# Performance work log

Hardware: AMD Instinct MI355X
Metric: run time of the kernel (lower is better)

Reference implementation:

```python
import jax, jax.numpy as jnp
import numpy as np

N, E = 50000, 800000          # nodes, edges
IN, H1, D1 = 128, 8, 32       # gcn1: 8 heads x 32 -> concat 256
HID1 = H1 * D1                # 256
HID2 = 128                    # gcn2: 1 head x 128
FC1, OUT = 512, 1
NEG_SLOPE = 0.2


def _nrm(k, shape, s=0.05):
    return jax.random.normal(k, shape, jnp.float32) * s


def setup_inputs() -> dict:
    key = jax.random.key(0)
    ks = jax.random.split(key, 16)
    return {
        "x": jax.random.normal(ks[0], (N, IN), jnp.float32),
        "edge_index": jax.random.randint(ks[1], (2, E), 0, N, dtype=jnp.int32),
        # gcn1 params
        "W1": _nrm(ks[2], (IN, H1 * D1)),
        "att_src1": _nrm(ks[3], (H1, D1)),
        "att_dst1": _nrm(ks[4], (H1, D1)),
        "b1": jnp.zeros((HID1,), jnp.float32),
        # gcn2 params (1 head)
        "W2": _nrm(ks[5], (HID1, HID2)),
        "att_src2": _nrm(ks[6], (1, HID2)),
        "att_dst2": _nrm(ks[7], (1, HID2)),
        "b2": jnp.zeros((HID2,), jnp.float32),
        # fc head
        "fcW1": _nrm(ks[8], (HID2, FC1)),
        "fcb1": jnp.zeros((FC1,), jnp.float32),
        "fcW2": _nrm(ks[9], (FC1, OUT)),
        "fcb2": jnp.zeros((OUT,), jnp.float32),
    }


def gat_layer(x, src, dst, W, a_src, a_dst, b, heads, dim):
    """PyG GATConv (eval mode): gather -> segment-softmax over dst -> scatter."""
    n = x.shape[0]
    h = (x @ W).reshape(n, heads, dim)                     # [N,H,D]
    a_s = jnp.einsum('nhd,hd->nh', h, a_src)               # [N,H]
    a_d = jnp.einsum('nhd,hd->nh', h, a_dst)
    e = jax.nn.leaky_relu(a_s[src] + a_d[dst], NEG_SLOPE)  # [E,H]
    m = jax.ops.segment_max(e, dst, num_segments=n)        # [N,H]
    m = jnp.where(jnp.isfinite(m), m, 0.0)                 # empty segments
    ex = jnp.exp(e - m[dst])
    denom = jax.ops.segment_sum(ex, dst, num_segments=n)
    alpha = ex / (denom[dst] + 1e-16)                      # [E,H]
    out = jax.ops.segment_sum(h[src] * alpha[:, :, None], dst, num_segments=n)
    return out.reshape(n, heads * dim) + b, alpha


def reference(x, edge_index, W1, att_src1, att_dst1, b1,
              W2, att_src2, att_dst2, b2, fcW1, fcb1, fcW2, fcb2):
    src, dst = edge_index[0], edge_index[1]
    x1, alpha1 = gat_layer(x, src, dst, W1, att_src1, att_dst1, b1, H1, D1)
    x1 = jax.nn.elu(x1)
    x2, alpha2 = gat_layer(x1, src, dst, W2, att_src2, att_dst2, b2, 1, HID2)
    x2 = jax.nn.relu(x2)
    h = jax.nn.relu(x2 @ fcW1 + fcb1)
    out = h @ fcW2 + fcb2                                  # [N,1]
    return out, alpha1, alpha2
```

## Files before the change

kernel.cpp:

```cpp
#include <hip/hip_runtime.h>
#include <hip/hip_bf16.h>
#include <hip/hip_fp8.h>
#include <math.h>

#define NN 50000
#define EE 800000
#define IN_DIM 128
#define H1 8
#define D1 32
#define HID1 256
#define HID2 128
#define FC1 512
#define NEG_SLOPE 0.2f

typedef short v8s __attribute__((ext_vector_type(8)));
typedef float v4f __attribute__((ext_vector_type(4)));
typedef float v2f __attribute__((ext_vector_type(2)));
typedef unsigned int v4u __attribute__((ext_vector_type(4)));

__device__ __forceinline__ float bf2f(unsigned short u) {
    unsigned int x = ((unsigned int)u) << 16;
    return __uint_as_float(x);
}
__device__ __forceinline__ unsigned short f2bf(float v) {
    __hip_bfloat16 h = __float2bfloat16(v);
    return *(unsigned short*)&h;
}
__device__ __forceinline__ unsigned char f2f8(float v) {
    __hip_fp8_e4m3 t(v);
    return (unsigned char)t.__x;
}
__device__ __forceinline__ float f8tof(unsigned char u) {
    __hip_fp8_e4m3 t;
    t.__x = (__hip_fp8_storage_t)u;
    return (float)t;
}

__device__ __forceinline__ void f8x4(unsigned int w, float& f0, float& f1, float& f2, float& f3) {
#if __has_builtin(__builtin_amdgcn_cvt_pk_f32_fp8)
    v2f lo = __builtin_amdgcn_cvt_pk_f32_fp8((int)w, false);
    v2f hi = __builtin_amdgcn_cvt_pk_f32_fp8((int)w, true);
    f0 = lo[0]; f1 = lo[1]; f2 = hi[0]; f3 = hi[1];
#else
    f0 = f8tof((unsigned char)(w & 0xff));
    f1 = f8tof((unsigned char)((w >> 8) & 0xff));
    f2 = f8tof((unsigned char)((w >> 16) & 0xff));
    f3 = f8tof((unsigned char)(w >> 24));
#endif
}


__global__ void hist_kernel(const int* __restrict__ dst, int* __restrict__ counts) {
    int e = blockIdx.x * blockDim.x + threadIdx.x;
    if (e < EE) atomicAdd(&counts[dst[e]], 1);
}

__global__ __launch_bounds__(256) void scan_a_kernel(const int* __restrict__ counts,
                                                     int* __restrict__ excl,
                                                     int* __restrict__ bsum, int n) {
    __shared__ int wsum[4];
    int tid = threadIdx.x;
    int base = blockIdx.x * 1024 + tid * 4;
    int v0 = 0, v1 = 0, v2 = 0, v3 = 0;
    if (base + 3 < n) {
        int4 t = *(const int4*)(counts + base);
        v0 = t.x; v1 = t.y; v2 = t.z; v3 = t.w;
    } else {
        if (base + 0 < n) v0 = counts[base + 0];
        if (base + 1 < n) v1 = counts[base + 1];
        if (base + 2 < n) v2 = counts[base + 2];
        if (base + 3 < n) v3 = counts[base + 3];
    }
    int tot = v0 + v1 + v2 + v3;
    int lane = tid & 63;
    int w = tid >> 6;
    int x = tot;
    #pragma unroll
    for (int off = 1; off < 64; off <<= 1) {
        int y = __shfl_up(x, off);
        if (lane >= off) x += y;
    }
    if (lane == 63) wsum[w] = x;
    __syncthreads();
    int woff = 0;
    for (int i = 0; i < w; i++) woff += wsum[i];
    int et = woff + x - tot;
    if (base + 0 < n) excl[base + 0] = et;
    if (base + 1 < n) excl[base + 1] = et + v0;
    if (base + 2 < n) excl[base + 2] = et + v0 + v1;
    if (base + 3 < n) excl[base + 3] = et + v0 + v1 + v2;
    if (tid == 255) bsum[blockIdx.x] = woff + x;
}

__global__ __launch_bounds__(64) void scan_b_kernel(int* __restrict__ bsum,
                                                    int* __restrict__ row_ptr, int nb, int n) {
    int lane = threadIdx.x;
    int v = (lane < nb) ? bsum[lane] : 0;
    int x = v;
    #pragma unroll
    for (int off = 1; off < 64; off <<= 1) {
        int y = __shfl_up(x, off);
        if (lane >= off) x += y;
    }
    if (lane < nb) bsum[lane] = x - v;
    if (lane == 63) row_ptr[n] = x;
}

__global__ __launch_bounds__(256) void scan_c_kernel(const int* __restrict__ excl,
                                                     const int* __restrict__ bsum,
                                                     int* __restrict__ row_ptr,
                                                     int* __restrict__ cursor, int n) {
    int base = blockIdx.x * 1024 + threadIdx.x * 4;
    int off = bsum[blockIdx.x];
    #pragma unroll
    for (int j = 0; j < 4; j++) {
        int i = base + j;
        if (i < n) {
            int r = excl[i] + off;
            row_ptr[i] = r;
            cursor[i] = r;
        }
    }
}

__global__ void scatter_kernel(const int* __restrict__ src, const int* __restrict__ dst,
                               int* __restrict__ cursor, int2* __restrict__ pairs) {
    int e = blockIdx.x * blockDim.x + threadIdx.x;
    if (e >= EE) return;
    int d = dst[e];
    int p = atomicAdd(&cursor[d], 1);
    pairs[p] = make_int2(e, src[e]);
}


__device__ __forceinline__ void pack_one(const float* __restrict__ B,
                                         __hip_bfloat16* __restrict__ Bp,
                                         int K, int N, int idx) {
    int k = idx / N, n = idx % N;
    int ntile = n >> 4, ks = k >> 5, kk = k & 31;
    int lane = (n & 15) | ((kk >> 3) << 4);
    int j = kk & 7;
    int KS = K >> 5;
    Bp[((size_t)(ntile * KS + ks) * 64 + lane) * 8 + j] = __float2bfloat16(B[idx]);
}

__global__ void prep_kernel(const float* __restrict__ x, __hip_bfloat16* __restrict__ xbf,
                            const float* __restrict__ W1, __hip_bfloat16* __restrict__ W1p,
                            const float* __restrict__ W2, __hip_bfloat16* __restrict__ W2p,
                            const float* __restrict__ fcW1, __hip_bfloat16* __restrict__ fW1p) {
    int i = blockIdx.x * blockDim.x + threadIdx.x;
    const int N0 = NN * IN_DIM;
    const int N1 = N0 + IN_DIM * HID1;
    const int N2 = N1 + HID1 * HID2;
    const int N3 = N2 + HID2 * FC1;
    if (i < N0) xbf[i] = __float2bfloat16(x[i]);
    else if (i < N1) pack_one(W1, W1p, IN_DIM, HID1, i - N0);
    else if (i < N2) pack_one(W2, W2p, HID1, HID2, i - N1);
    else if (i < N3) pack_one(fcW1, fW1p, HID2, FC1, i - N2);
}


template <int ATT>
__global__ __launch_bounds__(256) void mgemm_kernel(const __hip_bfloat16* __restrict__ A,
                                                    const __hip_bfloat16* __restrict__ Bp,
                                                    unsigned char* __restrict__ Cf8,
                                                    const float* __restrict__ as_w,
                                                    const float* __restrict__ ad_w,
                                                    float* __restrict__ a_s,
                                                    float* __restrict__ a_d,
                                                    int M, int K, int N) {
    int w = threadIdx.x >> 6, l = threadIdx.x & 63;
    int bm = blockIdx.x * 128 + w * 32;
    int bn = blockIdx.y * 64;
    int lr = l & 15, lk = l >> 4;
    int KS = K >> 5;
    const short* Ab = (const short*)A;
    const short* Bb = (const short*)Bp;
    v4f acc[2][4];
    #pragma unroll
    for (int mi = 0; mi < 2; mi++)
        #pragma unroll
        for (int nt = 0; nt < 4; nt++) acc[mi][nt] = (v4f)(0.f);
    for (int ks = 0; ks < KS; ks++) {
        v8s a[2];
        #pragma unroll
        for (int mi = 0; mi < 2; mi++) {
            int gm = bm + mi * 16 + lr;
            a[mi] = (gm < M) ? *(const v8s*)(Ab + (size_t)gm * K + ks * 32 + lk * 8)
                             : (v8s)(short)0;
        }
        #pragma unroll
        for (int nt = 0; nt < 4; nt++) {
            int ntile = (bn >> 4) + nt;
            v8s b = *(const v8s*)(Bb + ((size_t)(ntile * KS + ks) * 64 + l) * 8);
            acc[0][nt] = __builtin_amdgcn_mfma_f32_16x16x32_bf16(a[0], b, acc[0][nt], 0, 0, 0);
            acc[1][nt] = __builtin_amdgcn_mfma_f32_16x16x32_bf16(a[1], b, acc[1][nt], 0, 0, 0);
        }
    }
    #pragma unroll
    for (int mi = 0; mi < 2; mi++) {
        #pragma unroll
        for (int nt = 0; nt < 4; nt++) {
            int gn = bn + nt * 16 + lr;
            #pragma unroll
            for (int j = 0; j < 4; j++) {
                int gm = bm + mi * 16 + lk * 4 + j;
                if (gm < M)
                    Cf8[(size_t)gm * N + gn] = f2f8(acc[mi][nt][j]);
            }
        }
    }
    float ws0 = as_w[bn + lr], ws1 = as_w[bn + 16 + lr];
    float ws2 = as_w[bn + 32 + lr], ws3 = as_w[bn + 48 + lr];
    float wd0 = ad_w[bn + lr], wd1 = ad_w[bn + 16 + lr];
    float wd2 = ad_w[bn + 32 + lr], wd3 = ad_w[bn + 48 + lr];
    float sA[2][4], dA[2][4], sB[2][4], dB[2][4];
    #pragma unroll
    for (int mi = 0; mi < 2; mi++)
        #pragma unroll
        for (int j = 0; j < 4; j++) {
            if constexpr (ATT == 1) {
                sA[mi][j] = acc[mi][0][j] * ws0 + acc[mi][1][j] * ws1;
                sB[mi][j] = acc[mi][2][j] * ws2 + acc[mi][3][j] * ws3;
                dA[mi][j] = acc[mi][0][j] * wd0 + acc[mi][1][j] * wd1;
                dB[mi][j] = acc[mi][2][j] * wd2 + acc[mi][3][j] * wd3;
            } else {
                sA[mi][j] = acc[mi][0][j] * ws0 + acc[mi][1][j] * ws1
                          + acc[mi][2][j] * ws2 + acc[mi][3][j] * ws3;
                dA[mi][j] = acc[mi][0][j] * wd0 + acc[mi][1][j] * wd1
                          + acc[mi][2][j] * wd2 + acc[mi][3][j] * wd3;
                sB[mi][j] = 0.f; dB[mi][j] = 0.f;
            }
        }
    #pragma unroll
    for (int off = 1; off < 16; off <<= 1) {
        #pragma unroll
        for (int mi = 0; mi < 2; mi++)
            #pragma unroll
            for (int j = 0; j < 4; j++) {
                sA[mi][j] += __shfl_xor(sA[mi][j], off);
                dA[mi][j] += __shfl_xor(dA[mi][j], off);
                if constexpr (ATT == 1) {
                    sB[mi][j] += __shfl_xor(sB[mi][j], off);
                    dB[mi][j] += __shfl_xor(dB[mi][j], off);
                }
            }
    }
    if (lr == 0) {
        #pragma unroll
        for (int mi = 0; mi < 2; mi++)
            #pragma unroll
            for (int j = 0; j < 4; j++) {
                int row = bm + mi * 16 + lk * 4 + j;
                if (row < M) {
                    if constexpr (ATT == 1) {
                        int h0 = bn >> 5;
                        a_s[(size_t)row * 8 + h0]     = sA[mi][j];
                        a_s[(size_t)row * 8 + h0 + 1] = sB[mi][j];
                        a_d[(size_t)row * 8 + h0]     = dA[mi][j];
                        a_d[(size_t)row * 8 + h0 + 1] = dB[mi][j];
                    } else {
                        atomicAdd(&a_s[row], sA[mi][j]);
                        atomicAdd(&a_d[row], dA[mi][j]);
                    }
                }
            }
    }
}


__global__ __launch_bounds__(256) void fc_mfma_kernel(const __hip_bfloat16* __restrict__ A,
                                                      const __hip_bfloat16* __restrict__ Bp,
                                                      const float* __restrict__ fcb1,
                                                      const float* __restrict__ fcW2,
                                                      const float* __restrict__ fcb2,
                                                      float* __restrict__ out) {
    __shared__ float red[4][32];
    int w = threadIdx.x >> 6, l = threadIdx.x & 63;
    int bm = blockIdx.x * 32;
    int lr = l & 15, lk = l >> 4;
    const int K = HID2, KS = K >> 5;
    const short* Ab = (const short*)A;
    const short* Bb = (const short*)Bp;
    v4f acc[2][8];
    #pragma unroll
    for (int mi = 0; mi < 2; mi++)
        #pragma unroll
        for (int nt = 0; nt < 8; nt++) acc[mi][nt] = (v4f)(0.f);
    for (int ks = 0; ks < KS; ks++) {
        v8s a[2];
        #pragma unroll
        for (int mi = 0; mi < 2; mi++) {
            int gm = bm + mi * 16 + lr;
            a[mi] = (gm < NN) ? *(const v8s*)(Ab + (size_t)gm * K + ks * 32 + lk * 8)
                              : (v8s)(short)0;
        }
        #pragma unroll
        for (int nt = 0; nt < 8; nt++) {
            int ntile = w * 8 + nt;
            v8s b = *(const v8s*)(Bb + ((size_t)(ntile * KS + ks) * 64 + l) * 8);
            acc[0][nt] = __builtin_amdgcn_mfma_f32_16x16x32_bf16(a[0], b, acc[0][nt], 0, 0, 0);
            acc[1][nt] = __builtin_amdgcn_mfma_f32_16x16x32_bf16(a[1], b, acc[1][nt], 0, 0, 0);
        }
    }
    float p[2][4];
    #pragma unroll
    for (int mi = 0; mi < 2; mi++)
        #pragma unroll
        for (int j = 0; j < 4; j++) p[mi][j] = 0.f;
    #pragma unroll
    for (int nt = 0; nt < 8; nt++) {
        int col = w * 128 + nt * 16 + lr;
        float b1v = fcb1[col], w2v = fcW2[col];
        #pragma unroll
        for (int mi = 0; mi < 2; mi++) {
            #pragma unroll
            for (int j = 0; j < 4; j++) {
                float v = acc[mi][nt][j] + b1v;
                p[mi][j] += ((v > 0.f) ? v : 0.f) * w2v;
            }
        }
    }
    #pragma unroll
    for (int mi = 0; mi < 2; mi++)
        #pragma unroll
        for (int j = 0; j < 4; j++) {
            float v = p[mi][j];
            v += __shfl_xor(v, 1);
            v += __shfl_xor(v, 2);
            v += __shfl_xor(v, 4);
            v += __shfl_xor(v, 8);
            p[mi][j] = v;
        }
    if (lr == 0) {
        #pragma unroll
        for (int mi = 0; mi < 2; mi++)
            #pragma unroll
            for (int j = 0; j < 4; j++) red[w][mi * 16 + lk * 4 + j] = p[mi][j];
    }
    __syncthreads();
    int tid = threadIdx.x;
    if (tid < 32) {
        int gm = bm + tid;
        if (gm < NN)
            out[gm] = red[0][tid] + red[1][tid] + red[2][tid] + red[3][tid] + fcb2[0];
    }
}


template <int KM>
__device__ __forceinline__ void gat1_fast(int lane, int start, int cnt,
                                          const int2* __restrict__ pairs,
                                          const float* __restrict__ a_s, float ad,
                                          const unsigned char* __restrict__ hf8,
                                          float* __restrict__ alpha1_out,
                                          float& acc0, float& acc1, float& acc2, float& acc3) {
    int h = lane & 7, j = lane >> 3;
    int hl = lane >> 3;
    int cl = min(lane, cnt - 1);
    int2 ep = pairs[start + cl];
    int e_all = ep.x, s_all = ep.y;
    unsigned int loff = (unsigned int)(lane << 2);

    if constexpr (KM <= 4) {
        constexpr int NB = KM * 8;
        int sj[KM];
        float ev[KM];
        #pragma unroll
        for (int k = 0; k < KM; k++) {
            int idx = j + k * 8;
            sj[k] = __shfl(s_all, idx);
            ev[k] = a_s[(size_t)sj[k] * 8 + h];
        }
        unsigned int qt[NB];
        #pragma unroll
        for (int e = 0; e < NB; e++) {
            int sje = __shfl(s_all, e);
            qt[e] = *(const unsigned int*)(hf8 + (((unsigned int)sje << 8) | loff));
        }
        float ex[KM];
        #pragma unroll
        for (int k = 0; k < KM; k++) {
            int idx = j + k * 8;
            float v = ev[k] + ad;
            v = (v >= 0.f) ? v : NEG_SLOPE * v;
            ex[k] = (idx < cnt) ? v : -INFINITY;
        }
        float m = ex[0];
        #pragma unroll
        for (int k = 1; k < KM; k++) m = fmaxf(m, ex[k]);
        m = fmaxf(m, __shfl_xor(m, 8));
        m = fmaxf(m, __shfl_xor(m, 16));
        m = fmaxf(m, __shfl_xor(m, 32));
        float s = 0.f;
        #pragma unroll
        for (int k = 0; k < KM; k++) {
            ex[k] = expf(ex[k] - m);
            s += ex[k];
        }
        s += __shfl_xor(s, 8);
        s += __shfl_xor(s, 16);
        s += __shfl_xor(s, 32);
        float inv = 1.f / (s + 1e-16f);
        #pragma unroll
        for (int k = 0; k < KM; k++) ex[k] *= inv;
        #pragma unroll
        for (int k = 0; k < KM; k++) {
            int idx = j + k * 8;
            int eo = __shfl(e_all, idx);
            if (idx < cnt) alpha1_out[(size_t)eo * 8 + h] = ex[k];
        }
        #pragma unroll
        for (int e = 0; e < NB; e++) {
            float At = __shfl(ex[e >> 3], (e & 7) * 8 + hl);
            float f0, f1, f2, f3;
            f8x4(qt[e], f0, f1, f2, f3);
            acc0 += At * f0;
            acc1 += At * f1;
            acc2 += At * f2;
            acc3 += At * f3;
        }
    } else {
        float ex[KM];
        int sj[KM];
        #pragma unroll
        for (int k = 0; k < KM; k++) {
            int idx = j + k * 8;
            sj[k] = __shfl(s_all, idx);
            float v = a_s[(size_t)sj[k] * 8 + h] + ad;
            v = (v >= 0.f) ? v : NEG_SLOPE * v;
            ex[k] = (idx < cnt) ? v : -INFINITY;
        }
        float m = ex[0];
        #pragma unroll
        for (int k = 1; k < KM; k++) m = fmaxf(m, ex[k]);
        m = fmaxf(m, __shfl_xor(m, 8));
        m = fmaxf(m, __shfl_xor(m, 16));
        m = fmaxf(m, __shfl_xor(m, 32));
        float s = 0.f;
        #pragma unroll
        for (int k = 0; k < KM; k++) {
            ex[k] = expf(ex[k] - m);
            s += ex[k];
        }
        s += __shfl_xor(s, 8);
        s += __shfl_xor(s, 16);
        s += __shfl_xor(s, 32);
        float inv = 1.f / (s + 1e-16f);
        #pragma unroll
        for (int k = 0; k < KM; k++) ex[k] *= inv;
        #pragma unroll
        for (int k = 0; k < KM; k++) {
            int idx = j + k * 8;
            int eo = __shfl(e_all, idx);
            if (idx < cnt) alpha1_out[(size_t)eo * 8 + h] = ex[k];
        }
        unsigned int pk[KM];
        #pragma unroll
        for (int k = 0; k < KM; k++)
            pk[k] = ((unsigned int)sj[k] << 16) | (unsigned int)f2bf(ex[k]);
        int rounds = (cnt + 7) >> 3;
        #pragma unroll
        for (int K = 0; K < KM; K++) {
            if (K < rounds) {
                float At[8];
                unsigned int qt[8];
                #pragma unroll
                for (int t = 0; t < 8; t++) {
                    unsigned int wv = (unsigned int)__shfl((int)pk[K], t * 8 + hl);
                    At[t] = bf2f((unsigned short)wv);
                    qt[t] = *(const unsigned int*)(hf8 + (((wv >> 16) << 8) | loff));
                }
                #pragma unroll
                for (int t = 0; t < 8; t++) {
                    float f0, f1, f2, f3;
                    f8x4(qt[t], f0, f1, f2, f3);
                    acc0 += At[t] * f0;
                    acc1 += At[t] * f1;
                    acc2 += At[t] * f2;
                    acc3 += At[t] * f3;
                }
            }
        }
    }
}

__global__ __launch_bounds__(256) void gat1_kernel(const int* __restrict__ row_ptr,
                                                   const int2* __restrict__ pairs,
                                                   const float* __restrict__ a_s,
                                                   const float* __restrict__ a_d,
                                                   const unsigned char* __restrict__ h1f8,
                                                   const float* __restrict__ b1,
                                                   float* __restrict__ alpha1_out,
                                                   __hip_bfloat16* __restrict__ x1bf) {
    int wv = threadIdx.x >> 6, lane = threadIdx.x & 63;
    int n = blockIdx.x * 4 + wv;
    if (n >= NN) return;
    int start = row_ptr[n], end = row_ptr[n + 1];
    int cnt = end - start;
    int h = lane & 7, j = lane >> 3;
    int hl = lane >> 3;
    unsigned int loff = (unsigned int)(lane << 2);
    float acc0 = 0.f, acc1 = 0.f, acc2 = 0.f, acc3 = 0.f;
    if (cnt > 0 && cnt <= 64) {
        float ad = a_d[(size_t)n * 8 + h];
        if (cnt <= 8)
            gat1_fast<1>(lane, start, cnt, pairs, a_s, ad, h1f8, alpha1_out, acc0, acc1, acc2, acc3);
        else if (cnt <= 16)
            gat1_fast<2>(lane, start, cnt, pairs, a_s, ad, h1f8, alpha1_out, acc0, acc1, acc2, acc3);
        else if (cnt <= 24)
            gat1_fast<3>(lane, start, cnt, pairs, a_s, ad, h1f8, alpha1_out, acc0, acc1, acc2, acc3);
        else if (cnt <= 32)
            gat1_fast<4>(lane, start, cnt, pairs, a_s, ad, h1f8, alpha1_out, acc0, acc1, acc2, acc3);
        else
            gat1_fast<8>(lane, start, cnt, pairs, a_s, ad, h1f8, alpha1_out, acc0, acc1, acc2, acc3);
    } else if (cnt > 64) {
        float ad = a_d[(size_t)n * 8 + h];
        float m = -INFINITY;
        for (int p = start + j; p < end; p += 8) {
            float v = a_s[(size_t)pairs[p].y * 8 + h] + ad;
            v = (v >= 0.f) ? v : NEG_SLOPE * v;
            m = fmaxf(m, v);
        }
        m = fmaxf(m, __shfl_xor(m, 8));
        m = fmaxf(m, __shfl_xor(m, 16));
        m = fmaxf(m, __shfl_xor(m, 32));
        float s = 0.f;
        for (int p = start + j; p < end; p += 8) {
            float v = a_s[(size_t)pairs[p].y * 8 + h] + ad;
            v = (v >= 0.f) ? v : NEG_SLOPE * v;
            s += expf(v - m);
        }
        s += __shfl_xor(s, 8);
        s += __shfl_xor(s, 16);
        s += __shfl_xor(s, 32);
        float inv = 1.f / (s + 1e-16f);
        for (int p = start + j; p < end; p += 8) {
            int2 ep = pairs[p];
            float v = a_s[(size_t)ep.y * 8 + h] + ad;
            v = (v >= 0.f) ? v : NEG_SLOPE * v;
            alpha1_out[(size_t)ep.x * 8 + h] = expf(v - m) * inv;
        }
        float mh = __shfl(m, hl);
        float invh = __shfl(inv, hl);
        float adh = __shfl(ad, hl);
        for (int p = start; p < end; p++) {
            int sp = pairs[p].y;
            float v = a_s[(size_t)sp * 8 + hl] + adh;
            v = (v >= 0.f) ? v : NEG_SLOPE * v;
            float al = expf(v - mh) * invh;
            unsigned int q = *(const unsigned int*)(h1f8 + (((unsigned int)sp << 8) | loff));
            float f0, f1, f2, f3;
            f8x4(q, f0, f1, f2, f3);
            acc0 += al * f0;
            acc1 += al * f1;
            acc2 += al * f2;
            acc3 += al * f3;
        }
    }
    float4 bb = *(const float4*)(b1 + lane * 4);
    float r0 = acc0 + bb.x, r1 = acc1 + bb.y, r2 = acc2 + bb.z, r3 = acc3 + bb.w;
    r0 = (r0 > 0.f) ? r0 : expf(r0) - 1.f;
    r1 = (r1 > 0.f) ? r1 : expf(r1) - 1.f;
    r2 = (r2 > 0.f) ? r2 : expf(r2) - 1.f;
    r3 = (r3 > 0.f) ? r3 : expf(r3) - 1.f;
    ushort4 o;
    o.x = f2bf(r0); o.y = f2bf(r1); o.z = f2bf(r2); o.w = f2bf(r3);
    *(ushort4*)((unsigned short*)x1bf + (size_t)n * HID1 + lane * 4) = o;
}


template <int RM>
__device__ __forceinline__ void gat2_fast(int lane, int start, int cnt, int r, int c,
                                          const int2* __restrict__ pairs,
                                          const float* __restrict__ a_s, float ad,
                                          const unsigned char* __restrict__ hf8,
                                          float* __restrict__ alpha2_out,
                                          float& acc0, float& acc1, float& acc2, float& acc3) {
    bool act = lane < cnt;
    int ii = min(lane, cnt - 1);
    int2 ep = pairs[start + ii];
    int sj = ep.y;
    float asv = a_s[sj];
    unsigned int coff = (unsigned int)(c << 2);
    constexpr int NB = RM * 4;
    unsigned int qt[NB];
    #pragma unroll
    for (int t = 0; t < NB; t++) {
        int je = (t >> 2) * 8 + (t & 3) * 2 + r;
        int sje = __shfl(sj, je);
        qt[t] = *(const unsigned int*)(hf8 + (((unsigned int)sje << 7) | coff));
    }
    float v = asv + ad;
    v = (v >= 0.f) ? v : NEG_SLOPE * v;
    float e = act ? v : -INFINITY;
    float m = e;
    #pragma unroll
    for (int off = 1; off < 64; off <<= 1) m = fmaxf(m, __shfl_xor(m, off));
    float ex = expf(e - m);
    float s = ex;
    #pragma unroll
    for (int off = 1; off < 64; off <<= 1) s += __shfl_xor(s, off);
    float al = ex / (s + 1e-16f);
    if (act) alpha2_out[ep.x] = al;
    #pragma unroll
    for (int t = 0; t < NB; t++) {
        int je = (t >> 2) * 8 + (t & 3) * 2 + r;
        float At = __shfl(al, je);
        float f0, f1, f2, f3;
        f8x4(qt[t], f0, f1, f2, f3);
        acc0 += At * f0;
        acc1 += At * f1;
        acc2 += At * f2;
        acc3 += At * f3;
    }
}

__global__ __launch_bounds__(256) void gat2_kernel(const int* __restrict__ row_ptr,
                                                   const int2* __restrict__ pairs,
                                                   const float* __restrict__ a_s,
                                                   const float* __restrict__ a_d,
                                                   const unsigned char* __restrict__ h2f8,
                                                   const float* __restrict__ b2,
                                                   float* __restrict__ alpha2_out,
                                                   __hip_bfloat16* __restrict__ x2bf) {
    int wv = threadIdx.x >> 6, lane = threadIdx.x & 63;
    int n = blockIdx.x * 4 + wv;
    if (n >= NN) return;
    int start = row_ptr[n], end = row_ptr[n + 1];
    int cnt = end - start;
    int r = lane >> 5, c = lane & 31;
    float acc0 = 0.f, acc1 = 0.f, acc2 = 0.f, acc3 = 0.f;
    if (cnt > 0 && cnt <= 64) {
        float ad = a_d[n];
        if (cnt <= 8)
            gat2_fast<1>(lane, start, cnt, r, c, pairs, a_s, ad, h2f8, alpha2_out, acc0, acc1, acc2, acc3);
        else if (cnt <= 16)
            gat2_fast<2>(lane, start, cnt, r, c, pairs, a_s, ad, h2f8, alpha2_out, acc0, acc1, acc2, acc3);
        else if (cnt <= 32)
            gat2_fast<4>(lane, start, cnt, r, c, pairs, a_s, ad, h2f8, alpha2_out, acc0, acc1, acc2, acc3);
        else
            gat2_fast<8>(lane, start, cnt, r, c, pairs, a_s, ad, h2f8, alpha2_out, acc0, acc1, acc2, acc3);
    } else if (cnt > 64) {
        float ad = a_d[n];
        unsigned int coff = (unsigned int)(c << 2);
        float m = -INFINITY;
        for (int p = start + lane; p < end; p += 64) {
            float v = a_s[pairs[p].y] + ad;
            v = (v >= 0.f) ? v : NEG_SLOPE * v;
            m = fmaxf(m, v);
        }
        for (int off = 32; off; off >>= 1) m = fmaxf(m, __shfl_xor(m, off));
        float s = 0.f;
        for (int p = start + lane; p < end; p += 64) {
            float v = a_s[pairs[p].y] + ad;
            v = (v >= 0.f) ? v : NEG_SLOPE * v;
            s += expf(v - m);
        }
        for (int off = 32; off; off >>= 1) s += __shfl_xor(s, off);
        float inv = 1.f / (s + 1e-16f);
        for (int p = start + lane; p < end; p += 64) {
            int2 ep = pairs[p];
            float v = a_s[ep.y] + ad;
            v = (v >= 0.f) ? v : NEG_SLOPE * v;
            alpha2_out[ep.x] = expf(v - m) * inv;
        }
        for (int p = start + r; p < end; p += 2) {
            int sp = pairs[p].y;
            float v = a_s[sp] + ad;
            v = (v >= 0.f) ? v : NEG_SLOPE * v;
            float al = expf(v - m) * inv;
            unsigned int q = *(const unsigned int*)(h2f8 + (((unsigned int)sp << 7) | coff));
            float f0, f1, f2, f3;
            f8x4(q, f0, f1, f2, f3);
            acc0 += al * f0;
            acc1 += al * f1;
            acc2 += al * f2;
            acc3 += al * f3;
        }
    }
    acc0 += __shfl_xor(acc0, 32);
    acc1 += __shfl_xor(acc1, 32);
    acc2 += __shfl_xor(acc2, 32);
    acc3 += __shfl_xor(acc3, 32);
    if (r == 0) {
        float4 bb = *(const float4*)(b2 + c * 4);
        float r0 = acc0 + bb.x, r1 = acc1 + bb.y, r2 = acc2 + bb.z, r3 = acc3 + bb.w;
        r0 = (r0 > 0.f) ? r0 : 0.f;
        r1 = (r1 > 0.f) ? r1 : 0.f;
        r2 = (r2 > 0.f) ? r2 : 0.f;
        r3 = (r3 > 0.f) ? r3 : 0.f;
        ushort4 o;
        o.x = f2bf(r0); o.y = f2bf(r1); o.z = f2bf(r2); o.w = f2bf(r3);
        *(ushort4*)((unsigned short*)x2bf + (size_t)n * HID2 + c * 4) = o;
    }
}


extern "C" void kernel_launch(void* const* d_in, const int* in_sizes, int n_in,
                              void* d_out, int out_size, void* d_ws, size_t ws_size,
                              hipStream_t stream) {
    (void)in_sizes; (void)n_in; (void)out_size; (void)ws_size;
    const float* x        = (const float*)d_in[0];
    const int*   eindex   = (const int*)d_in[1];
    const float* W1       = (const float*)d_in[2];
    const float* att_src1 = (const float*)d_in[3];
    const float* att_dst1 = (const float*)d_in[4];
    const float* b1       = (const float*)d_in[5];
    const float* W2       = (const float*)d_in[6];
    const float* att_src2 = (const float*)d_in[7];
    const float* att_dst2 = (const float*)d_in[8];
    const float* b2       = (const float*)d_in[9];
    const float* fcW1     = (const float*)d_in[10];
    const float* fcb1     = (const float*)d_in[11];
    const float* fcW2     = (const float*)d_in[12];
    const float* fcb2     = (const float*)d_in[13];

    const int* src = eindex;
    const int* dst = eindex + EE;

    float* out_n      = (float*)d_out;
    float* alpha1_out = out_n + NN;
    float* alpha2_out = alpha1_out + (size_t)EE * 8;

    char* ws = (char*)d_ws;
    size_t off = 0;
    auto alloc = [&](size_t bytes) {
        size_t o = off;
        off = (off + bytes + 255) & ~(size_t)255;
        return o;
    };
    size_t o_rowptr = alloc((NN + 1) * sizeof(int));
    size_t o_cursor = alloc(NN * sizeof(int));
    size_t o_counts = alloc(NN * sizeof(int));
    size_t o_excl   = alloc(NN * sizeof(int));
    size_t o_bsum   = alloc(64 * sizeof(int));
    size_t o_pairs  = alloc((size_t)EE * sizeof(int2));
    size_t o_as1    = alloc((size_t)NN * H1 * sizeof(float));
    size_t o_ad1    = alloc((size_t)NN * H1 * sizeof(float));
    size_t o_as2    = alloc((size_t)NN * sizeof(float));
    size_t o_ad2    = alloc((size_t)NN * sizeof(float));
    size_t o_h1f8   = alloc((size_t)NN * HID1);
    size_t o_xbf    = alloc((size_t)NN * IN_DIM * sizeof(__hip_bfloat16));
    size_t o_x1bf   = alloc((size_t)NN * HID1 * sizeof(__hip_bfloat16));
    size_t o_h2f8   = alloc((size_t)NN * HID2);
    size_t o_x2bf   = alloc((size_t)NN * HID2 * sizeof(__hip_bfloat16));
    size_t o_W1p    = alloc((size_t)IN_DIM * HID1 * sizeof(__hip_bfloat16));
    size_t o_W2p    = alloc((size_t)HID1 * HID2 * sizeof(__hip_bfloat16));
    size_t o_fW1p   = alloc((size_t)HID2 * FC1 * sizeof(__hip_bfloat16));

    int*   row_ptr = (int*)(ws + o_rowptr);
    int*   cursor  = (int*)(ws + o_cursor);
    int*   counts  = (int*)(ws + o_counts);
    int*   excl    = (int*)(ws + o_excl);
    int*   bsum    = (int*)(ws + o_bsum);
    int2*  pairs   = (int2*)(ws + o_pairs);
    float* a_s1    = (float*)(ws + o_as1);
    float* a_d1    = (float*)(ws + o_ad1);
    float* a_s2    = (float*)(ws + o_as2);
    float* a_d2    = (float*)(ws + o_ad2);
    unsigned char*  h1f8  = (unsigned char*)(ws + o_h1f8);
    __hip_bfloat16* xbf   = (__hip_bfloat16*)(ws + o_xbf);
    __hip_bfloat16* x1bf  = (__hip_bfloat16*)(ws + o_x1bf);
    unsigned char*  h2f8  = (unsigned char*)(ws + o_h2f8);
    __hip_bfloat16* x2bf  = (__hip_bfloat16*)(ws + o_x2bf);
    __hip_bfloat16* W1p   = (__hip_bfloat16*)(ws + o_W1p);
    __hip_bfloat16* W2p   = (__hip_bfloat16*)(ws + o_W2p);
    __hip_bfloat16* fW1p  = (__hip_bfloat16*)(ws + o_fW1p);

    const int SCAN_NB = (NN + 1023) / 1024;
    const int PREP_N = NN * IN_DIM + IN_DIM * HID1 + HID1 * HID2 + HID2 * FC1;

    hipMemsetAsync(counts, 0, NN * sizeof(int), stream);
    hipMemsetAsync(a_s2, 0, NN * sizeof(float), stream);
    hipMemsetAsync(a_d2, 0, NN * sizeof(float), stream);

    hist_kernel<<<(EE + 255) / 256, 256, 0, stream>>>(dst, counts);
    scan_a_kernel<<<SCAN_NB, 256, 0, stream>>>(counts, excl, bsum, NN);
    scan_b_kernel<<<1, 64, 0, stream>>>(bsum, row_ptr, SCAN_NB, NN);
    scan_c_kernel<<<SCAN_NB, 256, 0, stream>>>(excl, bsum, row_ptr, cursor, NN);
    scatter_kernel<<<(EE + 255) / 256, 256, 0, stream>>>(src, dst, cursor, pairs);

    prep_kernel<<<(PREP_N + 255) / 256, 256, 0, stream>>>(x, xbf, W1, W1p, W2, W2p, fcW1, fW1p);

    mgemm_kernel<1><<<dim3((NN + 127) / 128, HID1 / 64), 256, 0, stream>>>(
        xbf, W1p, h1f8, att_src1, att_dst1, a_s1, a_d1, NN, IN_DIM, HID1);
    gat1_kernel<<<(NN + 3) / 4, 256, 0, stream>>>(row_ptr, pairs, a_s1, a_d1,
                                                  h1f8, b1, alpha1_out, x1bf);

    mgemm_kernel<2><<<dim3((NN + 127) / 128, HID2 / 64), 256, 0, stream>>>(
        x1bf, W2p, h2f8, att_src2, att_dst2, a_s2, a_d2, NN, HID1, HID2);
    gat2_kernel<<<(NN + 3) / 4, 256, 0, stream>>>(row_ptr, pairs, a_s2, a_d2,
                                                  h2f8, b2, alpha2_out, x2bf);

    fc_mfma_kernel<<<(NN + 31) / 32, 256, 0, stream>>>(x2bf, fW1p, fcb1, fcW2, fcb2, out_n);
}
```

Measured before the change: 264.5 us.

## Replicate histogram and scatter cursors across 16 copies to cut atomic contention

The degree histogram and the CSR scatter cursors are split into 16 replicas chosen by block index. A reduce kernel sums the replicas before the scan, and a base kernel turns per-replica counts into per-replica starting offsets. This is meant to spread same-address atomics and reduce contention during hist and scatter. In exchange it adds two kernel launches, a memset that is 16 times larger, and 3.2 MB of extra replica traffic. With random destinations there is little contention to begin with, so the gain may be small or negative.

Result: no change. 259.6 us (-1.8%).

```diff
diff --git a/kernel.cpp b/kernel.cpp
--- a/kernel.cpp
+++ b/kernel.cpp
@@ -12,6 +12,7 @@
 #define HID2 128
 #define FC1 512
 #define NEG_SLOPE 0.2f
+#define NREP 16
 
 typedef short v8s __attribute__((ext_vector_type(8)));
 typedef float v4f __attribute__((ext_vector_type(4)));
@@ -50,9 +51,20 @@
 }
 
 
-__global__ void hist_kernel(const int* __restrict__ dst, int* __restrict__ counts) {
+__global__ void hist_kernel(const int* __restrict__ dst, int* __restrict__ counts_rep) {
     int e = blockIdx.x * blockDim.x + threadIdx.x;
-    if (e < EE) atomicAdd(&counts[dst[e]], 1);
+    if (e >= EE) return;
+    int r = blockIdx.x & (NREP - 1);
+    atomicAdd(&counts_rep[r * NN + dst[e]], 1);
+}
+
+__global__ void reduce_kernel(const int* __restrict__ counts_rep, int* __restrict__ counts_total) {
+    int d = blockIdx.x * blockDim.x + threadIdx.x;
+    if (d >= NN) return;
+    int t = 0;
+    #pragma unroll
+    for (int r = 0; r < NREP; r++) t += counts_rep[r * NN + d];
+    counts_total[d] = t;
 }
 
 __global__ __launch_bounds__(256) void scan_a_kernel(const int* __restrict__ counts,
@@ -108,27 +120,35 @@
 
 __global__ __launch_bounds__(256) void scan_c_kernel(const int* __restrict__ excl,
                                                      const int* __restrict__ bsum,
-                                                     int* __restrict__ row_ptr,
-                                                     int* __restrict__ cursor, int n) {
+                                                     int* __restrict__ row_ptr, int n) {
     int base = blockIdx.x * 1024 + threadIdx.x * 4;
     int off = bsum[blockIdx.x];
     #pragma unroll
     for (int j = 0; j < 4; j++) {
         int i = base + j;
-        if (i < n) {
-            int r = excl[i] + off;
-            row_ptr[i] = r;
-            cursor[i] = r;
-        }
+        if (i < n) row_ptr[i] = excl[i] + off;
+    }
+}
+
+__global__ void base_kernel(const int* __restrict__ row_ptr, const int* __restrict__ counts_rep,
+                            int* __restrict__ cursor_rep) {
+    int d = blockIdx.x * blockDim.x + threadIdx.x;
+    if (d >= NN) return;
+    int running = row_ptr[d];
+    #pragma unroll
+    for (int r = 0; r < NREP; r++) {
+        cursor_rep[r * NN + d] = running;
+        running += counts_rep[r * NN + d];
     }
 }
 
 __global__ void scatter_kernel(const int* __restrict__ src, const int* __restrict__ dst,
-                               int* __restrict__ cursor, int2* __restrict__ pairs) {
+                               int* __restrict__ cursor_rep, int2* __restrict__ pairs) {
     int e = blockIdx.x * blockDim.x + threadIdx.x;
     if (e >= EE) return;
+    int r = blockIdx.x & (NREP - 1);
     int d = dst[e];
-    int p = atomicAdd(&cursor[d], 1);
+    int p = atomicAdd(&cursor_rep[r * NN + d], 1);
     pairs[p] = make_int2(e, src[e]);
 }
 
@@ -731,8 +751,9 @@
         return o;
     };
     size_t o_rowptr = alloc((NN + 1) * sizeof(int));
-    size_t o_cursor = alloc(NN * sizeof(int));
-    size_t o_counts = alloc(NN * sizeof(int));
+    size_t o_crep   = alloc((size_t)NREP * NN * sizeof(int));
+    size_t o_curs   = alloc((size_t)NREP * NN * sizeof(int));
+    size_t o_ctot   = alloc(NN * sizeof(int));
     size_t o_excl   = alloc(NN * sizeof(int));
     size_t o_bsum   = alloc(64 * sizeof(int));
     size_t o_pairs  = alloc((size_t)EE * sizeof(int2));
@@ -749,16 +770,17 @@
     size_t o_W2p    = alloc((size_t)HID1 * HID2 * sizeof(__hip_bfloat16));
     size_t o_fW1p   = alloc((size_t)HID2 * FC1 * sizeof(__hip_bfloat16));
 
-    int*   row_ptr = (int*)(ws + o_rowptr);
-    int*   cursor  = (int*)(ws + o_cursor);
-    int*   counts  = (int*)(ws + o_counts);
-    int*   excl    = (int*)(ws + o_excl);
-    int*   bsum    = (int*)(ws + o_bsum);
-    int2*  pairs   = (int2*)(ws + o_pairs);
-    float* a_s1    = (float*)(ws + o_as1);
-    float* a_d1    = (float*)(ws + o_ad1);
-    float* a_s2    = (float*)(ws + o_as2);
-    float* a_d2    = (float*)(ws + o_ad2);
+    int*   row_ptr    = (int*)(ws + o_rowptr);
+    int*   counts_rep = (int*)(ws + o_crep);
+    int*   cursor_rep = (int*)(ws + o_curs);
+    int*   counts_tot = (int*)(ws + o_ctot);
+    int*   excl       = (int*)(ws + o_excl);
+    int*   bsum       = (int*)(ws + o_bsum);
+    int2*  pairs      = (int2*)(ws + o_pairs);
+    float* a_s1       = (float*)(ws + o_as1);
+    float* a_d1       = (float*)(ws + o_ad1);
+    float* a_s2       = (float*)(ws + o_as2);
+    float* a_d2       = (float*)(ws + o_ad2);
     unsigned char*  h1f8  = (unsigned char*)(ws + o_h1f8);
     __hip_bfloat16* xbf   = (__hip_bfloat16*)(ws + o_xbf);
     __hip_bfloat16* x1bf  = (__hip_bfloat16*)(ws + o_x1bf);
@@ -771,15 +793,17 @@
     const int SCAN_NB = (NN + 1023) / 1024;
     const int PREP_N = NN * IN_DIM + IN_DIM * HID1 + HID1 * HID2 + HID2 * FC1;
 
-    hipMemsetAsync(counts, 0, NN * sizeof(int), stream);
+    hipMemsetAsync(counts_rep, 0, (size_t)NREP * NN * sizeof(int), stream);
     hipMemsetAsync(a_s2, 0, NN * sizeof(float), stream);
     hipMemsetAsync(a_d2, 0, NN * sizeof(float), stream);
 
-    hist_kernel<<<(EE + 255) / 256, 256, 0, stream>>>(dst, counts);
-    scan_a_kernel<<<SCAN_NB, 256, 0, stream>>>(counts, excl, bsum, NN);
+    hist_kernel<<<(EE + 255) / 256, 256, 0, stream>>>(dst, counts_rep);
+    reduce_kernel<<<(NN + 255) / 256, 256, 0, stream>>>(counts_rep, counts_tot);
+    scan_a_kernel<<<SCAN_NB, 256, 0, stream>>>(counts_tot, excl, bsum, NN);
     scan_b_kernel<<<1, 64, 0, stream>>>(bsum, row_ptr, SCAN_NB, NN);
-    scan_c_kernel<<<SCAN_NB, 256, 0, stream>>>(excl, bsum, row_ptr, cursor, NN);
-    scatter_kernel<<<(EE + 255) / 256, 256, 0, stream>>>(src, dst, cursor, pairs);
+    scan_c_kernel<<<SCAN_NB, 256, 0, stream>>>(excl, bsum, row_ptr, NN);
+    base_kernel<<<(NN + 255) / 256, 256, 0, stream>>>(row_ptr, counts_rep, cursor_rep);
+    scatter_kernel<<<(EE + 255) / 256, 256, 0, stream>>>(src, dst, cursor_rep, pairs);
 
     prep_kernel<<<(PREP_N + 255) / 256, 256, 0, stream>>>(x, xbf, W1, W1p, W2, W2p, fcW1, fW1p);
 
```
